# Kernel optimization log

Measured on AMD Instinct MI355X. Metric: run time of the kernel, lower is better.

The kernel has to match this reference:

```python
import jax, jax.numpy as jnp
import numpy as np
from jax import lax

N, D, H, C = 4096, 1024, 512, 21  # rois, head feat dim, gcn hidden, n_classes


def setup_inputs() -> dict:
    key = jax.random.key(0)
    ks = jax.random.split(key, 9)
    x1 = jax.random.uniform(ks[0], (N,), minval=0.0, maxval=800.0)
    y1 = jax.random.uniform(ks[1], (N,), minval=0.0, maxval=800.0)
    w = jax.random.uniform(ks[2], (N,), minval=16.0, maxval=256.0)
    h = jax.random.uniform(ks[3], (N,), minval=16.0, maxval=256.0)
    rois = jnp.stack([x1, y1, x1 + w, y1 + h], axis=1)  # [N,4] x1,y1,x2,y2
    pooled_feat = jax.random.normal(ks[4], (N, D))
    Wg1 = jax.random.normal(ks[5], (D, H)) * 0.02
    bg1 = jnp.zeros((H,), jnp.float32)
    Wg2 = jax.random.normal(ks[6], (H, H)) * 0.02
    bg2 = jnp.zeros((H,), jnp.float32)
    W_bbox = jax.random.normal(ks[7], (H, 4 * C)) * 0.001
    b_bbox = jnp.zeros((4 * C,), jnp.float32)
    W_cls = jax.random.normal(ks[8], (H, C)) * 0.01
    b_cls = jnp.zeros((C,), jnp.float32)
    return dict(rois=rois, pooled_feat=pooled_feat, Wg1=Wg1, bg1=bg1, Wg2=Wg2,
                bg2=bg2, W_bbox=W_bbox, b_bbox=b_bbox, W_cls=W_cls, b_cls=b_cls)


def _iou_binary_adj(boxes):
    # bbox_overlaps_batch IoU (Pascal +1 convention), then binarize and zero diag
    x1, y1, x2, y2 = boxes[:, 0], boxes[:, 1], boxes[:, 2], boxes[:, 3]
    area = (x2 - x1 + 1.0) * (y2 - y1 + 1.0)
    iw = jnp.maximum(jnp.minimum(x2[:, None], x2[None, :]) - jnp.maximum(x1[:, None], x1[None, :]) + 1.0, 0.0)
    ih = jnp.maximum(jnp.minimum(y2[:, None], y2[None, :]) - jnp.maximum(y1[:, None], y1[None, :]) + 1.0, 0.0)
    inter = iw * ih
    iou = inter / (area[:, None] + area[None, :] - inter)
    adj = (iou > 0.0).astype(boxes.dtype)
    return adj * (1.0 - jnp.eye(boxes.shape[0], dtype=boxes.dtype))


def _connected_components(adj):
    # jit-friendly replacement for DFS subgraph_split: min-label propagation
    # with pointer jumping (converges in O(log diameter) iterations).
    n = adj.shape[0]
    labels0 = jnp.arange(n, dtype=jnp.int32)
    big = jnp.int32(n)

    def step(labels, _):
        nb = jnp.min(jnp.where(adj > 0.0, labels[None, :], big), axis=1)
        labels = jnp.minimum(labels, nb)
        labels = labels[labels]  # pointer jump
        return labels, None

    labels, _ = lax.scan(step, labels0, None, length=32)
    return labels  # component id per roi (min vertex index in component)


def _cosine_adj(x):
    # pairwise cosine similarity, diag zeroed (matches s != t loop)
    xn = x / jnp.maximum(jnp.linalg.norm(x, axis=1, keepdims=True), 1e-6)
    a = xn @ xn.T
    return a * (1.0 - jnp.eye(x.shape[0], dtype=x.dtype))


def reference(rois, pooled_feat, Wg1, bg1, Wg2, bg2, W_bbox, b_bbox, W_cls, b_cls):
    adj_bin = _iou_binary_adj(rois)          # [N,N] 0/1
    labels = _connected_components(adj_bin)  # [N] int32 subgraph ids
    A = _cosine_adj(pooled_feat)             # [N,N]
    h1 = jax.nn.relu(A @ (pooled_feat @ Wg1) + bg1)  # GCN layer 1
    h2 = jax.nn.relu(A @ (h1 @ Wg2) + bg2)           # GCN layer 2
    bbox_pred = h2 @ W_bbox + b_bbox          # [N, 4*C]
    cls_prob = jax.nn.softmax(h2 @ W_cls + b_cls, axis=1)  # [N, C]
    return labels, cls_prob, bbox_pred
```

## Files before the change

### kernel.cpp

```cpp
#include <hip/hip_runtime.h>
#include <hip/hip_bf16.h>
#include <stdint.h>


typedef __attribute__((ext_vector_type(8))) short short8;
typedef __attribute__((ext_vector_type(4))) float floatx4;

#define BK 64
#define LSTR 72

__device__ __forceinline__ unsigned short bfbits(float f) {
  union { float f; unsigned int i; } u; u.f = f;
  unsigned int r = u.i + 0x7fffu + ((u.i >> 16) & 1);
  return (unsigned short)(r >> 16);
}

__device__ __forceinline__ void minprop_node(const unsigned long long* adj, int* labels,
                                             int node, int lane) {
  unsigned long long w = adj[(size_t)node * 64 + lane];
  int m = 0x7fffffff;
  while (w) {
    int b = __builtin_ctzll(w);
    w &= w - 1;
    m = min(m, labels[lane * 64 + b]);
  }
  for (int o = 32; o; o >>= 1) m = min(m, __shfl_down(m, o));
  if (lane == 0 && m < labels[node]) atomicMin(&labels[node], m);
}

template <int MODE, int CC = 0>
__global__ __launch_bounds__(256) void gemm64(
    const __hip_bfloat16* __restrict__ P, const __hip_bfloat16* __restrict__ Q,
    int KC, int ld, int N, float* __restrict__ part,
    const float* __restrict__ rinorm, const __hip_bfloat16* __restrict__ ST,
    const float* __restrict__ bias, __hip_bfloat16* __restrict__ outb,
    float* __restrict__ outf, float* __restrict__ cls, const float* __restrict__ bias2,
    const int* __restrict__ labelsIn, float* __restrict__ outL) {
  __shared__ short As[2][64 * LSTR];
  __shared__ short Bs[2][64 * LSTR];
  const int tid = threadIdx.x;

  if (CC == 1 && blockIdx.y == 8) {
    int i = blockIdx.x * 256 + tid;
    if (i < 4096) {
      int l = labelsIn[i];
      int p = labelsIn[l];
      while (p != l) { l = p; p = labelsIn[l]; }
      outL[i] = (float)l;
    }
    return;
  }

  const int w = tid >> 6, lane = tid & 63;
  const size_t m0 = (size_t)blockIdx.y * 64, n0 = (size_t)blockIdx.x * 64;
  const int z = blockIdx.z;

  const int srow = tid >> 2, skoff = (tid & 3) * 16;
  const short* gA = (const short*)P + (m0 + srow) * (size_t)ld + (size_t)z * KC + skoff;
  const short* gB = (const short*)Q + (n0 + srow) * (size_t)ld + (size_t)z * KC + skoff;
  const int soff = srow * LSTR + skoff;

  const int wm = (w >> 1) * 32, wn = (w & 1) * 32;
  const int lr = lane & 15, ko = (lane >> 4) * 8;

  floatx4 acc[2][2];
#pragma unroll
  for (int i = 0; i < 2; ++i)
#pragma unroll
    for (int j = 0; j < 2; ++j) acc[i][j] = (floatx4){0.f, 0.f, 0.f, 0.f};

  const int nIter = KC / BK;
  short8 ra0 = *(const short8*)gA;
  short8 ra1 = *(const short8*)(gA + 8);
  short8 rb0 = *(const short8*)gB;
  short8 rb1 = *(const short8*)(gB + 8);
  *(short8*)&As[0][soff] = ra0;
  *(short8*)&As[0][soff + 8] = ra1;
  *(short8*)&Bs[0][soff] = rb0;
  *(short8*)&Bs[0][soff + 8] = rb1;
  if (nIter > 1) {
    ra0 = *(const short8*)(gA + BK);
    ra1 = *(const short8*)(gA + BK + 8);
    rb0 = *(const short8*)(gB + BK);
    rb1 = *(const short8*)(gB + BK + 8);
  }
  __syncthreads();

  for (int it = 0; it < nIter; ++it) {
    const int cur = it & 1;
    short8 av[2][2], bv[2][2];
#pragma unroll
    for (int ks = 0; ks < 2; ++ks)
#pragma unroll
      for (int t = 0; t < 2; ++t) {
        av[ks][t] = *(const short8*)&As[cur][(wm + t * 16 + lr) * LSTR + ks * 32 + ko];
        bv[ks][t] = *(const short8*)&Bs[cur][(wn + t * 16 + lr) * LSTR + ks * 32 + ko];
      }
    if (it + 1 < nIter) {
      *(short8*)&As[cur ^ 1][soff] = ra0;
      *(short8*)&As[cur ^ 1][soff + 8] = ra1;
      *(short8*)&Bs[cur ^ 1][soff] = rb0;
      *(short8*)&Bs[cur ^ 1][soff + 8] = rb1;
      if (it + 2 < nIter) {
        const int off = (it + 2) * BK;
        ra0 = *(const short8*)(gA + off);
        ra1 = *(const short8*)(gA + off + 8);
        rb0 = *(const short8*)(gB + off);
        rb1 = *(const short8*)(gB + off + 8);
      }
    }
#pragma unroll
    for (int ks = 0; ks < 2; ++ks)
#pragma unroll
      for (int i = 0; i < 2; ++i)
#pragma unroll
        for (int j = 0; j < 2; ++j)
          acc[i][j] = __builtin_amdgcn_mfma_f32_16x16x32_bf16(av[ks][i], bv[ks][j], acc[i][j], 0, 0, 0);
    __syncthreads();
  }

  const size_t MN = (size_t)8 * 64 * (size_t)N;
  float* cp = part + (size_t)z * MN;
  float* lg = (float*)&As[0][0];
  const int rb4 = (lane >> 4) * 4;
#pragma unroll
  for (int i = 0; i < 2; ++i)
#pragma unroll
    for (int j = 0; j < 2; ++j)
#pragma unroll
      for (int r = 0; r < 4; ++r) {
        int row = (int)m0 + wm + i * 16 + rb4 + r;
        int col = (int)n0 + wn + j * 16 + lr;
        float v = acc[i][j][r];
        if (MODE == 0) {
          cp[(size_t)row * N + col] = v;
        } else if (MODE == 1) {
          outb[(size_t)row * 4096 + col] = __float2bfloat16(v);
        } else if (MODE == 2) {
          v = rinorm[row] * v - __bfloat162float(ST[(size_t)col * 4096 + row]) + bias[col];
          outb[(size_t)row * 512 + col] = __float2bfloat16(fmaxf(v, 0.f));
        } else {
          if (blockIdx.x == 0) {
            outf[(size_t)row * 84 + col] = v + bias[col];
          } else {
            int lrow = wm + i * 16 + rb4 + r;
            if (col < 84) outf[(size_t)row * 84 + col] = v + bias[col];
            else if (col < 105) lg[lrow * 22 + (col - 84)] = v + bias2[col - 84];
          }
        }
      }
  if (MODE == 3) {
    __syncthreads();
    if (blockIdx.x == 1 && tid < 64) {
      const float* Lr = &lg[tid * 22];
      float m = Lr[0];
#pragma unroll
      for (int k = 1; k < 21; ++k) m = fmaxf(m, Lr[k]);
      float s = 0.f;
      float e[21];
#pragma unroll
      for (int k = 0; k < 21; ++k) { e[k] = expf(Lr[k] - m); s += e[k]; }
      float inv = 1.f / s;
      float* dst = &cls[(m0 + tid) * 21];
#pragma unroll
      for (int k = 0; k < 21; ++k) dst[k] = e[k] * inv;
    }
  }
}

__global__ void k_red0(const float* __restrict__ part, __hip_bfloat16* __restrict__ out,
                       int n, int ns) {
  int i = (blockIdx.x * 256 + threadIdx.x) * 4;
  if (i >= n) return;
  float4 v = *(const float4*)(part + i);
  for (int s = 1; s < ns; ++s) {
    float4 q = *(const float4*)(part + (size_t)s * n + i);
    v.x += q.x; v.y += q.y; v.z += q.z; v.w += q.w;
  }
  out[i] = __float2bfloat16(v.x);
  out[i + 1] = __float2bfloat16(v.y);
  out[i + 2] = __float2bfloat16(v.z);
  out[i + 3] = __float2bfloat16(v.w);
}

__global__ void k_nf_adj(const float* __restrict__ X, __hip_bfloat16* __restrict__ Xb,
                         float* __restrict__ rinorm, const float4* __restrict__ rois,
                         unsigned long long* __restrict__ adj, int* __restrict__ labels) {
  int blk = blockIdx.x, tid = threadIdx.x;
  int lane = tid & 63;
  if (blk < 1024) {
    int wave = (blk * 256 + tid) >> 6;
    const float4* row = (const float4*)(X + (size_t)wave * 1024);
    uint2* orow = (uint2*)((short*)Xb + (size_t)wave * 1024);
    float s = 0.f;
#pragma unroll
    for (int it = 0; it < 4; ++it) {
      float4 p = row[lane + it * 64];
      s += p.x * p.x + p.y * p.y + p.z * p.z + p.w * p.w;
      uint2 q;
      q.x = (unsigned int)bfbits(p.x) | ((unsigned int)bfbits(p.y) << 16);
      q.y = (unsigned int)bfbits(p.z) | ((unsigned int)bfbits(p.w) << 16);
      orow[lane + it * 64] = q;
    }
    for (int o = 32; o; o >>= 1) s += __shfl_down(s, o);
    if (lane == 0) rinorm[wave] = 1.f / fmaxf(sqrtf(s), 1e-6f);
  } else {
    int node = ((blk - 1024) * 256 + tid) >> 6;
    float4 bi = rois[node];
    unsigned long long myword = 0;
    int mn = node;
    for (int w = 0; w < 64; ++w) {
      int j = w * 64 + lane;
      float4 bj = rois[j];
      float iw = fminf(bi.z, bj.z) - fmaxf(bi.x, bj.x) + 1.0f;
      float ih = fminf(bi.w, bj.w) - fmaxf(bi.y, bj.y) + 1.0f;
      bool ov = (iw > 0.f) && (ih > 0.f) && (j != node);
      unsigned long long msk = __ballot(ov);
      if (lane == w) myword = msk;
      if (msk) mn = min(mn, w * 64 + (int)__builtin_ctzll(msk));
    }
    adj[(size_t)node * 64 + lane] = myword;
    if (lane == 0) labels[node] = mn;
  }
}

__global__ void k_prep(const __hip_bfloat16* __restrict__ Xb, const float* __restrict__ rinorm,
                       const float* __restrict__ Wg1, const float* __restrict__ Wg2,
                       const float* __restrict__ Wb, const float* __restrict__ Wc,
                       __hip_bfloat16* __restrict__ XRT, __hip_bfloat16* __restrict__ Wg1T,
                       __hip_bfloat16* __restrict__ Wg2T, __hip_bfloat16* __restrict__ WcatT,
                       const unsigned long long* __restrict__ adj, int* __restrict__ labels) {
  __shared__ float s[32][33];
  const int tid = threadIdx.x;
  const int tx = tid & 31, ty = tid >> 5;
  int blk = blockIdx.x;
  if (blk < 4096) {
    int c0 = (blk & 31) * 32, r0 = (blk >> 5) * 32;
#pragma unroll
    for (int k = 0; k < 4; ++k) {
      int r = r0 + ty + k * 8;
      s[ty + k * 8][tx] = __bfloat162float(Xb[(size_t)r * 1024 + c0 + tx]) * rinorm[r];
    }
    __syncthreads();
#pragma unroll
    for (int k = 0; k < 4; ++k)
      XRT[(size_t)(c0 + ty + k * 8) * 4096 + r0 + tx] = __float2bfloat16(s[tx][ty + k * 8]);
  } else if (blk < 4608) {
    int l = blk - 4096;
    int c0 = (l & 15) * 32, r0 = (l >> 4) * 32;
#pragma unroll
    for (int k = 0; k < 4; ++k)
      s[ty + k * 8][tx] = Wg1[(size_t)(r0 + ty + k * 8) * 512 + c0 + tx];
    __syncthreads();
#pragma unroll
    for (int k = 0; k < 4; ++k)
      Wg1T[(size_t)(c0 + ty + k * 8) * 1024 + r0 + tx] = __float2bfloat16(s[tx][ty + k * 8]);
  } else if (blk < 4864) {
    int l = blk - 4608;
    int c0 = (l & 15) * 32, r0 = (l >> 4) * 32;
#pragma unroll
    for (int k = 0; k < 4; ++k)
      s[ty + k * 8][tx] = Wg2[(size_t)(r0 + ty + k * 8) * 512 + c0 + tx];
    __syncthreads();
#pragma unroll
    for (int k = 0; k < 4; ++k)
      Wg2T[(size_t)(c0 + ty + k * 8) * 512 + r0 + tx] = __float2bfloat16(s[tx][ty + k * 8]);
  } else if (blk < 5120) {
    int idx = (blk - 4864) * 256 + tid;
    int r = idx >> 9, k = idx & 511;
    float v = 0.f;
    if (r < 84) v = Wb[(size_t)k * 84 + r];
    else if (r < 105) v = Wc[(size_t)k * 21 + (r - 84)];
    WcatT[idx] = __float2bfloat16(v);
  } else {
    int node = (blk - 5120) * 4 + (tid >> 6);
    minprop_node(adj, labels, node, tid & 63);
  }
}

__global__ void k_minprop(const unsigned long long* __restrict__ adj, int* __restrict__ labels) {
  int wave = (blockIdx.x * 256 + threadIdx.x) >> 6;
  minprop_node(adj, labels, wave, threadIdx.x & 63);
}

extern "C" void kernel_launch(void* const* d_in, const int* in_sizes, int n_in,
                              void* d_out, int out_size, void* d_ws, size_t ws_size,
                              hipStream_t stream) {
  const float* rois = (const float*)d_in[0];
  const float* X    = (const float*)d_in[1];
  const float* Wg1  = (const float*)d_in[2];
  const float* bg1  = (const float*)d_in[3];
  const float* Wg2  = (const float*)d_in[4];
  const float* bg2  = (const float*)d_in[5];
  const float* Wb   = (const float*)d_in[6];
  const float* bb   = (const float*)d_in[7];
  const float* Wc   = (const float*)d_in[8];
  const float* bc   = (const float*)d_in[9];

  float* out        = (float*)d_out;
  float* out_labels = out;
  float* out_cls    = out + 4096;
  float* out_bbox   = out + 4096 + 4096 * 21;

  char* p = (char*)d_ws;
  auto carve = [&](size_t bytes) { char* r = p; p += (bytes + 255) & ~(size_t)255; return r; };
  int* labels           = (int*)carve(4096ull * 4);
  float* rinorm         = (float*)carve(4096ull * 4);
  __hip_bfloat16* WcatT = (__hip_bfloat16*)carve(128ull * 512 * 2);
  __hip_bfloat16* Wg2T  = (__hip_bfloat16*)carve(512ull * 512 * 2);
  __hip_bfloat16* Wg1T  = (__hip_bfloat16*)carve(512ull * 1024 * 2);
  __hip_bfloat16* T2T   = (__hip_bfloat16*)carve(512ull * 1024 * 2);
  __hip_bfloat16* h     = (__hip_bfloat16*)carve(4096ull * 512 * 2);
  __hip_bfloat16* ST    = (__hip_bfloat16*)carve(512ull * 4096 * 2);
  __hip_bfloat16* Xb    = (__hip_bfloat16*)carve(4096ull * 1024 * 2);
  __hip_bfloat16* XRT   = (__hip_bfloat16*)carve(1024ull * 4096 * 2);
  unsigned long long* adj = (unsigned long long*)carve(4096ull * 64 * 8);
  float* part           = (float*)carve(16ull * 1024 * 1024);

  k_nf_adj<<<2048, 256, 0, stream>>>(X, Xb, rinorm, (const float4*)rois, adj, labels);
  k_prep<<<6144, 256, 0, stream>>>(Xb, rinorm, Wg1, Wg2, Wb, Wc, XRT, Wg1T, Wg2T, WcatT,
                                   adj, labels);
  k_minprop<<<1024, 256, 0, stream>>>(adj, labels);

  gemm64<1, 1><<<dim3(64, 9), 256, 0, stream>>>(Wg1T, Xb, 1024, 1024, 4096, part,
                                                nullptr, nullptr, nullptr, ST,
                                                nullptr, nullptr, nullptr,
                                                labels, out_labels);
  gemm64<0><<<dim3(16, 8, 4), 256, 0, stream>>>(ST, XRT, 1024, 4096, 1024, part,
                                                nullptr, nullptr, nullptr, nullptr,
                                                nullptr, nullptr, nullptr,
                                                nullptr, nullptr);
  k_red0<<<512, 256, 0, stream>>>(part, T2T, 512 * 1024, 4);
  gemm64<2><<<dim3(8, 64), 256, 0, stream>>>(Xb, T2T, 1024, 1024, 512, part,
                                             rinorm, ST, bg1, h,
                                             nullptr, nullptr, nullptr,
                                             nullptr, nullptr);
  gemm64<1><<<dim3(64, 8), 256, 0, stream>>>(Wg2T, h, 512, 512, 4096, part,
                                             nullptr, nullptr, nullptr, ST,
                                             nullptr, nullptr, nullptr,
                                             nullptr, nullptr);
  gemm64<0><<<dim3(16, 8, 4), 256, 0, stream>>>(ST, XRT, 1024, 4096, 1024, part,
                                                nullptr, nullptr, nullptr, nullptr,
                                                nullptr, nullptr, nullptr,
                                                nullptr, nullptr);
  k_red0<<<512, 256, 0, stream>>>(part, T2T, 512 * 1024, 4);
  gemm64<2><<<dim3(8, 64), 256, 0, stream>>>(Xb, T2T, 1024, 1024, 512, part,
                                             rinorm, ST, bg2, h,
                                             nullptr, nullptr, nullptr,
                                             nullptr, nullptr);
  gemm64<3><<<dim3(2, 64), 256, 0, stream>>>(h, WcatT, 512, 512, 128, part,
                                             nullptr, nullptr, bb, nullptr,
                                             out_bbox, out_cls, bc,
                                             nullptr, nullptr);
}
```

Before: 199.6 us.

## Fold minprop passes into GEMM launches and regroup front prep kernels

Drops the standalone min-propagation kernel and runs that pass inside extra blocks of the first GEMM launch. The label pointer-jump finalisation moves into an extra block row of the following GEMM. The weight transposes move into the front adjacency/convert kernel, so the second prep kernel only does the X transpose plus one minprop pass. This cuts one launch and lets the graph work overlap with GEMM tiles. The trade-off is that minprop now reads labels while other blocks are still updating them, which relies on the monotone atomicMin updates still converging.

Result: slower. 210.0 us (+5.2%).

```diff
diff --git a/kernel.cpp b/kernel.cpp
--- a/kernel.cpp
+++ b/kernel.cpp
@@ -35,24 +35,32 @@
     const float* __restrict__ rinorm, const __hip_bfloat16* __restrict__ ST,
     const float* __restrict__ bias, __hip_bfloat16* __restrict__ outb,
     float* __restrict__ outf, float* __restrict__ cls, const float* __restrict__ bias2,
-    const int* __restrict__ labelsIn, float* __restrict__ outL) {
+    const unsigned long long* __restrict__ adj, int* __restrict__ labels,
+    float* __restrict__ outL) {
   __shared__ short As[2][64 * LSTR];
   __shared__ short Bs[2][64 * LSTR];
   const int tid = threadIdx.x;
-
-  if (CC == 1 && blockIdx.y == 8) {
-    int i = blockIdx.x * 256 + tid;
+  const int w = tid >> 6, lane = tid & 63;
+
+  if (CC == 1 && blockIdx.y < 4) {
+    int wv = (blockIdx.y * 64 + blockIdx.x) * 4 + w;
+#pragma unroll
+    for (int k = 0; k < 4; ++k) minprop_node(adj, labels, wv * 4 + k, lane);
+    return;
+  }
+  if (CC == 2 && blockIdx.y == 8) {
+    int i = (blockIdx.z * 16 + blockIdx.x) * 256 + tid;
     if (i < 4096) {
-      int l = labelsIn[i];
-      int p = labelsIn[l];
-      while (p != l) { l = p; p = labelsIn[l]; }
+      int l = labels[i];
+      int p = labels[l];
+      while (p != l) { l = p; p = labels[l]; }
       outL[i] = (float)l;
     }
     return;
   }
 
-  const int w = tid >> 6, lane = tid & 63;
-  const size_t m0 = (size_t)blockIdx.y * 64, n0 = (size_t)blockIdx.x * 64;
+  const size_t m0 = (size_t)(blockIdx.y - (CC == 1 ? 4 : 0)) * 64;
+  const size_t n0 = (size_t)blockIdx.x * 64;
   const int z = blockIdx.z;
 
   const int srow = tid >> 2, skoff = (tid & 3) * 16;
@@ -183,28 +191,34 @@
   out[i + 3] = __float2bfloat16(v.w);
 }
 
-__global__ void k_nf_adj(const float* __restrict__ X, __hip_bfloat16* __restrict__ Xb,
-                         float* __restrict__ rinorm, const float4* __restrict__ rois,
-                         unsigned long long* __restrict__ adj, int* __restrict__ labels) {
+__global__ void k_front(const float* __restrict__ X, __hip_bfloat16* __restrict__ Xb,
+                        float* __restrict__ rinorm, const float4* __restrict__ rois,
+                        unsigned long long* __restrict__ adj, int* __restrict__ labels,
+                        const float* __restrict__ Wg1, const float* __restrict__ Wg2,
+                        const float* __restrict__ Wb, const float* __restrict__ Wc,
+                        __hip_bfloat16* __restrict__ Wg1T, __hip_bfloat16* __restrict__ Wg2T,
+                        __hip_bfloat16* __restrict__ WcatT) {
+  __shared__ float s[32][33];
   int blk = blockIdx.x, tid = threadIdx.x;
   int lane = tid & 63;
+  const int tx = tid & 31, ty = tid >> 5;
   if (blk < 1024) {
     int wave = (blk * 256 + tid) >> 6;
     const float4* row = (const float4*)(X + (size_t)wave * 1024);
     uint2* orow = (uint2*)((short*)Xb + (size_t)wave * 1024);
-    float s = 0.f;
+    float sm = 0.f;
 #pragma unroll
     for (int it = 0; it < 4; ++it) {
       float4 p = row[lane + it * 64];
-      s += p.x * p.x + p.y * p.y + p.z * p.z + p.w * p.w;
+      sm += p.x * p.x + p.y * p.y + p.z * p.z + p.w * p.w;
       uint2 q;
       q.x = (unsigned int)bfbits(p.x) | ((unsigned int)bfbits(p.y) << 16);
       q.y = (unsigned int)bfbits(p.z) | ((unsigned int)bfbits(p.w) << 16);
       orow[lane + it * 64] = q;
     }
-    for (int o = 32; o; o >>= 1) s += __shfl_down(s, o);
-    if (lane == 0) rinorm[wave] = 1.f / fmaxf(sqrtf(s), 1e-6f);
-  } else {
+    for (int o = 32; o; o >>= 1) sm += __shfl_down(sm, o);
+    if (lane == 0) rinorm[wave] = 1.f / fmaxf(sqrtf(sm), 1e-6f);
+  } else if (blk < 2048) {
     int node = ((blk - 1024) * 256 + tid) >> 6;
     float4 bi = rois[node];
     unsigned long long myword = 0;
@@ -221,15 +235,39 @@
     }
     adj[(size_t)node * 64 + lane] = myword;
     if (lane == 0) labels[node] = mn;
-  }
-}
-
-__global__ void k_prep(const __hip_bfloat16* __restrict__ Xb, const float* __restrict__ rinorm,
-                       const float* __restrict__ Wg1, const float* __restrict__ Wg2,
-                       const float* __restrict__ Wb, const float* __restrict__ Wc,
-                       __hip_bfloat16* __restrict__ XRT, __hip_bfloat16* __restrict__ Wg1T,
-                       __hip_bfloat16* __restrict__ Wg2T, __hip_bfloat16* __restrict__ WcatT,
-                       const unsigned long long* __restrict__ adj, int* __restrict__ labels) {
+  } else if (blk < 2560) {
+    int l = blk - 2048;
+    int c0 = (l & 15) * 32, r0 = (l >> 4) * 32;
+#pragma unroll
+    for (int k = 0; k < 4; ++k)
+      s[ty + k * 8][tx] = Wg1[(size_t)(r0 + ty + k * 8) * 512 + c0 + tx];
+    __syncthreads();
+#pragma unroll
+    for (int k = 0; k < 4; ++k)
+      Wg1T[(size_t)(c0 + ty + k * 8) * 1024 + r0 + tx] = __float2bfloat16(s[tx][ty + k * 8]);
+  } else if (blk < 2816) {
+    int l = blk - 2560;
+    int c0 = (l & 15) * 32, r0 = (l >> 4) * 32;
+#pragma unroll
+    for (int k = 0; k < 4; ++k)
+      s[ty + k * 8][tx] = Wg2[(size_t)(r0 + ty + k * 8) * 512 + c0 + tx];
+    __syncthreads();
+#pragma unroll
+    for (int k = 0; k < 4; ++k)
+      Wg2T[(size_t)(c0 + ty + k * 8) * 512 + r0 + tx] = __float2bfloat16(s[tx][ty + k * 8]);
+  } else {
+    int idx = (blk - 2816) * 256 + tid;
+    int r = idx >> 9, k = idx & 511;
+    float v = 0.f;
+    if (r < 84) v = Wb[(size_t)k * 84 + r];
+    else if (r < 105) v = Wc[(size_t)k * 21 + (r - 84)];
+    WcatT[idx] = __float2bfloat16(v);
+  }
+}
+
+__global__ void k_prep2(const __hip_bfloat16* __restrict__ Xb, const float* __restrict__ rinorm,
+                        __hip_bfloat16* __restrict__ XRT,
+                        const unsigned long long* __restrict__ adj, int* __restrict__ labels) {
   __shared__ float s[32][33];
   const int tid = threadIdx.x;
   const int tx = tid & 31, ty = tid >> 5;
@@ -245,42 +283,10 @@
 #pragma unroll
     for (int k = 0; k < 4; ++k)
       XRT[(size_t)(c0 + ty + k * 8) * 4096 + r0 + tx] = __float2bfloat16(s[tx][ty + k * 8]);
-  } else if (blk < 4608) {
-    int l = blk - 4096;
-    int c0 = (l & 15) * 32, r0 = (l >> 4) * 32;
-#pragma unroll
-    for (int k = 0; k < 4; ++k)
-      s[ty + k * 8][tx] = Wg1[(size_t)(r0 + ty + k * 8) * 512 + c0 + tx];
-    __syncthreads();
-#pragma unroll
-    for (int k = 0; k < 4; ++k)
-      Wg1T[(size_t)(c0 + ty + k * 8) * 1024 + r0 + tx] = __float2bfloat16(s[tx][ty + k * 8]);
-  } else if (blk < 4864) {
-    int l = blk - 4608;
-    int c0 = (l & 15) * 32, r0 = (l >> 4) * 32;
-#pragma unroll
-    for (int k = 0; k < 4; ++k)
-      s[ty + k * 8][tx] = Wg2[(size_t)(r0 + ty + k * 8) * 512 + c0 + tx];
-    __syncthreads();
-#pragma unroll
-    for (int k = 0; k < 4; ++k)
-      Wg2T[(size_t)(c0 + ty + k * 8) * 512 + r0 + tx] = __float2bfloat16(s[tx][ty + k * 8]);
-  } else if (blk < 5120) {
-    int idx = (blk - 4864) * 256 + tid;
-    int r = idx >> 9, k = idx & 511;
-    float v = 0.f;
-    if (r < 84) v = Wb[(size_t)k * 84 + r];
-    else if (r < 105) v = Wc[(size_t)k * 21 + (r - 84)];
-    WcatT[idx] = __float2bfloat16(v);
   } else {
-    int node = (blk - 5120) * 4 + (tid >> 6);
+    int node = (blk - 4096) * 4 + (tid >> 6);
     minprop_node(adj, labels, node, tid & 63);
   }
-}
-
-__global__ void k_minprop(const unsigned long long* __restrict__ adj, int* __restrict__ labels) {
-  int wave = (blockIdx.x * 256 + threadIdx.x) >> 6;
-  minprop_node(adj, labels, wave, threadIdx.x & 63);
 }
 
 extern "C" void kernel_launch(void* const* d_in, const int* in_sizes, int n_in,
@@ -317,39 +323,38 @@
   unsigned long long* adj = (unsigned long long*)carve(4096ull * 64 * 8);
   float* part           = (float*)carve(16ull * 1024 * 1024);
 
-  k_nf_adj<<<2048, 256, 0, stream>>>(X, Xb, rinorm, (const float4*)rois, adj, labels);
-  k_prep<<<6144, 256, 0, stream>>>(Xb, rinorm, Wg1, Wg2, Wb, Wc, XRT, Wg1T, Wg2T, WcatT,
-                                   adj, labels);
-  k_minprop<<<1024, 256, 0, stream>>>(adj, labels);
-
-  gemm64<1, 1><<<dim3(64, 9), 256, 0, stream>>>(Wg1T, Xb, 1024, 1024, 4096, part,
-                                                nullptr, nullptr, nullptr, ST,
-                                                nullptr, nullptr, nullptr,
-                                                labels, out_labels);
-  gemm64<0><<<dim3(16, 8, 4), 256, 0, stream>>>(ST, XRT, 1024, 4096, 1024, part,
-                                                nullptr, nullptr, nullptr, nullptr,
-                                                nullptr, nullptr, nullptr,
-                                                nullptr, nullptr);
+  k_front<<<3072, 256, 0, stream>>>(X, Xb, rinorm, (const float4*)rois, adj, labels,
+                                    Wg1, Wg2, Wb, Wc, Wg1T, Wg2T, WcatT);
+  k_prep2<<<5120, 256, 0, stream>>>(Xb, rinorm, XRT, adj, labels);
+
+  gemm64<1, 1><<<dim3(64, 12), 256, 0, stream>>>(Wg1T, Xb, 1024, 1024, 4096, part,
+                                                 nullptr, nullptr, nullptr, ST,
+                                                 nullptr, nullptr, nullptr,
+                                                 adj, labels, nullptr);
+  gemm64<0, 2><<<dim3(16, 9, 4), 256, 0, stream>>>(ST, XRT, 1024, 4096, 1024, part,
+                                                   nullptr, nullptr, nullptr, nullptr,
+                                                   nullptr, nullptr, nullptr,
+                                                   nullptr, labels, out_labels);
   k_red0<<<512, 256, 0, stream>>>(part, T2T, 512 * 1024, 4);
   gemm64<2><<<dim3(8, 64), 256, 0, stream>>>(Xb, T2T, 1024, 1024, 512, part,
                                              rinorm, ST, bg1, h,
                                              nullptr, nullptr, nullptr,
-                                             nullptr, nullptr);
+                                             nullptr, nullptr, nullptr);
   gemm64<1><<<dim3(64, 8), 256, 0, stream>>>(Wg2T, h, 512, 512, 4096, part,
                                              nullptr, nullptr, nullptr, ST,
                                              nullptr, nullptr, nullptr,
-                                             nullptr, nullptr);
+                                             nullptr, nullptr, nullptr);
   gemm64<0><<<dim3(16, 8, 4), 256, 0, stream>>>(ST, XRT, 1024, 4096, 1024, part,
                                                 nullptr, nullptr, nullptr, nullptr,
                                                 nullptr, nullptr, nullptr,
-                                                nullptr, nullptr);
+                                                nullptr, nullptr, nullptr);
   k_red0<<<512, 256, 0, stream>>>(part, T2T, 512 * 1024, 4);
   gemm64<2><<<dim3(8, 64), 256, 0, stream>>>(Xb, T2T, 1024, 1024, 512, part,
                                              rinorm, ST, bg2, h,
                                              nullptr, nullptr, nullptr,
-                                             nullptr, nullptr);
+                                             nullptr, nullptr, nullptr);
   gemm64<3><<<dim3(2, 64), 256, 0, stream>>>(h, WcatT, 512, 512, 128, part,
                                              nullptr, nullptr, bb, nullptr,
                                              out_bbox, out_cls, bc,
-                                             nullptr, nullptr);
-}
+                                             nullptr, nullptr, nullptr);
+}
```
